# Performance work log

Hardware: AMD Instinct MI355X
Metric: run time of the kernel (lower is better)

The kernel has to match this reference:

```python
import jax, jax.numpy as jnp
import numpy as np

B, S, D, H, DFF = 4, 2048, 1024, 8, 4096
DH = D // H  # 128
EPS = 1e-5


def layernorm(x, gamma, beta):
    mu = jnp.mean(x, axis=-1, keepdims=True)
    var = jnp.mean(jnp.square(x - mu), axis=-1, keepdims=True)
    return (x - mu) * jax.lax.rsqrt(var + EPS) * gamma + beta


def setup_inputs() -> dict:
    key = jax.random.key(0)
    ks = jax.random.split(key, 6)
    s = 0.02
    return {
        "src": jax.random.normal(ks[0], (B, S, D), jnp.float32),
        "w_qkv": jax.random.normal(ks[1], (D, 3 * D), jnp.float32) * s,
        "w_out": jax.random.normal(ks[2], (D, D), jnp.float32) * s,
        "w1": jax.random.normal(ks[3], (D, DFF), jnp.float32) * s,
        "b1": jnp.zeros((DFF,), jnp.float32),
        "w2": jax.random.normal(ks[4], (DFF, D), jnp.float32) * s,
        "b2": jnp.zeros((D,), jnp.float32),
        "g1": jnp.ones((D,), jnp.float32),
        "beta1": jnp.zeros((D,), jnp.float32),
        "g2": jnp.ones((D,), jnp.float32),
        "beta2": jnp.zeros((D,), jnp.float32),
    }


def reference(src, w_qkv, w_out, w1, b1, w2, b2, g1, beta1, g2, beta2):
    b, s, d = src.shape
    # --- RingAttention == exact causal MHA on a single device ---
    qkv = src @ w_qkv  # [b, s, 3d]
    q, k, v = jnp.split(qkv, 3, axis=-1)
    to_heads = lambda x: x.reshape(b, s, H, DH).transpose(0, 2, 1, 3)  # [b,h,s,dh]
    q, k, v = to_heads(q), to_heads(k), to_heads(v)
    scale = 1.0 / jnp.sqrt(jnp.asarray(DH, src.dtype))
    scores = jnp.einsum('bhqd,bhkd->bhqk', q, k) * scale  # [b,h,s,s]
    causal = jnp.tril(jnp.ones((s, s), bool))
    neg = jnp.asarray(jnp.finfo(src.dtype).min, src.dtype)
    scores = jnp.where(causal, scores, neg)
    attn = jax.nn.softmax(scores, axis=-1)
    o = jnp.einsum('bhqk,bhkd->bhqd', attn, v)  # [b,h,s,dh]
    o = o.transpose(0, 2, 1, 3).reshape(b, s, d) @ w_out
    # dropout layers are identity at inference
    x = layernorm(src + o, g1, beta1)
    ff = jax.nn.relu(x @ w1 + b1) @ w2 + b2
    return layernorm(x + ff, g2, beta2)
```

## Files before the change

kernel.cpp:

```cpp
#include <hip/hip_runtime.h>

typedef unsigned short u16;
typedef __attribute__((ext_vector_type(8))) short short8;
typedef __attribute__((ext_vector_type(4))) float float4v;

#define MFMA_BF16(a, b, c) __builtin_amdgcn_mfma_f32_16x16x32_bf16((a), (b), (c), 0, 0, 0)

#define B_ 4
#define S_ 2048
#define D_ 1024
#define H_ 8
#define DH_ 128
#define DFF_ 4096
#define EPS_ 1e-5f
#define ROWS_ (B_ * S_)
#define CSCALE_ 0.12751672939502f

__device__ __forceinline__ u16 f2bf(float f) {
  union { float f; unsigned u; } x; x.f = f;
  unsigned r = x.u + 0x7fffu + ((x.u >> 16) & 1u);
  return (u16)(r >> 16);
}

typedef __attribute__((address_space(1))) const unsigned int guint;
typedef __attribute__((address_space(3))) unsigned int luint;
__device__ __forceinline__ void gl2lds16(const u16* g, u16* l) {
  __builtin_amdgcn_global_load_lds((guint*)g, (luint*)l, 16, 0, 0);
}

__device__ __forceinline__ size_t tiled_off(int row, int k, int Kdim) {
  return ((size_t)(row >> 7) * (Kdim >> 5) + (k >> 5)) * 4096 +
         (size_t)((row & 127) << 5) + (k & 31);
}

__global__ void cast_tiled_kernel(const float* __restrict__ in, u16* __restrict__ out) {
  int idx = blockIdx.x * 256 + threadIdx.x;
  int g = idx * 4;
  int m = g >> 10, k = g & 1023;
  float4 v = *(const float4*)(in + (size_t)g);
  ushort4 u;
  u.x = f2bf(v.x); u.y = f2bf(v.y); u.z = f2bf(v.z); u.w = f2bf(v.w);
  *(ushort4*)(out + tiled_off(m, k, D_)) = u;
}

__global__ void transpose_cast_kernel(const float* __restrict__ in, u16* __restrict__ out,
                                      int K, int N) {
  __shared__ float t[32][33];
  int k0 = blockIdx.x * 32, n0 = blockIdx.y * 32;
  int tx = threadIdx.x & 31, ty = threadIdx.x >> 5;
  #pragma unroll
  for (int i = 0; i < 4; ++i)
    t[ty + 8 * i][tx] = in[(size_t)(k0 + ty + 8 * i) * N + n0 + tx];
  __syncthreads();
  #pragma unroll
  for (int i = 0; i < 4; ++i)
    out[(size_t)(n0 + ty + 8 * i) * K + k0 + tx] = f2bf(t[tx][ty + 8 * i]);
}

__global__ void transpose_v_kernel(const u16* __restrict__ in, u16* __restrict__ out) {
  __shared__ u16 t[32][33];
  int s0 = blockIdx.x * 32, d0 = blockIdx.y * 32, bh = blockIdx.z;
  const u16* src = in + (size_t)bh * S_ * DH_;
  u16* dst = out + (size_t)bh * DH_ * S_;
  int tx = threadIdx.x & 31, ty = threadIdx.x >> 5;
  #pragma unroll
  for (int i = 0; i < 4; ++i)
    t[ty + 8 * i][tx] = src[(size_t)(s0 + ty + 8 * i) * DH_ + d0 + tx];
  __syncthreads();
  #pragma unroll
  for (int i = 0; i < 4; ++i)
    dst[(size_t)(d0 + ty + 8 * i) * S_ + s0 + tx] = t[tx][ty + 8 * i];
}

template <int MODE, int KT>
__global__ __launch_bounds__(256) void gemm_kernel(
    const u16* __restrict__ A, const u16* __restrict__ Bt,
    const int M, const int N,
    float* __restrict__ outF, u16* __restrict__ outH, const float* __restrict__ bias,
    const float* __restrict__ resid,
    u16* __restrict__ qo, u16* __restrict__ ko, u16* __restrict__ vo) {
  __shared__ u16 Bs[2][128][32];
  const int tid = threadIdx.x;
  const int lane = tid & 63, wave = tid >> 6;
  const int quad = lane >> 4, r16 = lane & 15;
  const int wm = (wave >> 1) * 64, wn = (wave & 1) * 64;
  const int m0 = blockIdx.x * 128, n0 = blockIdx.y * 128;
  constexpr int K = KT, niter = KT >> 5;

  float4v acc[4][4];
  #pragma unroll
  for (int i = 0; i < 4; ++i)
    #pragma unroll
    for (int j = 0; j < 4; ++j) acc[i][j] = (float4v)0.0f;

  const int drow = lane >> 2, dseg = lane & 3;
  const u16* Bg0 = Bt + (size_t)(n0 + wave * 32 + drow) * K + dseg * 8;
  const u16* Bg1 = Bg0 + (size_t)16 * K;
  u16* Bl0 = &Bs[0][wave * 32][0];
  u16* Bl1 = &Bs[0][wave * 32 + 16][0];
  constexpr int bufStep = 128 * 32;

  const u16* ap[4];
  #pragma unroll
  for (int t = 0; t < 4; ++t)
    ap[t] = A + (size_t)(m0 >> 7) * niter * 4096 +
            (size_t)((wm + t * 16 + r16) << 5) + quad * 8;

  gl2lds16(Bg0, Bl0);
  gl2lds16(Bg1, Bl1);
  short8 a_cur[4], a_nxt[4];
  #pragma unroll
  for (int t = 0; t < 4; ++t) a_cur[t] = *(const short8*)(ap[t]);

  #pragma unroll 2
  for (int i = 0; i < niter; ++i) {
    __syncthreads();
    if (i + 1 < niter) {
      const int k1 = (i + 1) << 5;
      const int bo = ((i + 1) & 1) ? bufStep : 0;
      gl2lds16(Bg0 + k1, Bl0 + bo);
      gl2lds16(Bg1 + k1, Bl1 + bo);
      const size_t o = (size_t)(i + 1) * 4096;
      #pragma unroll
      for (int t = 0; t < 4; ++t) a_nxt[t] = *(const short8*)(ap[t] + o);
    }
    short8 bfv[4];
    #pragma unroll
    for (int t = 0; t < 4; ++t)
      bfv[t] = *(const short8*)&Bs[i & 1][wn + t * 16 + r16][quad * 8];
    #pragma unroll
    for (int ii = 0; ii < 4; ++ii)
      #pragma unroll
      for (int j = 0; j < 4; ++j) acc[ii][j] = MFMA_BF16(a_cur[ii], bfv[j], acc[ii][j]);
    #pragma unroll
    for (int t = 0; t < 4; ++t) a_cur[t] = a_nxt[t];
  }

  #pragma unroll
  for (int i = 0; i < 4; ++i) {
    const int rowb = m0 + wm + i * 16 + quad * 4;
    #pragma unroll
    for (int j = 0; j < 4; ++j) {
      const int col = n0 + wn + j * 16 + r16;
      #pragma unroll
      for (int rg = 0; rg < 4; ++rg) {
        float val = acc[i][j][rg];
        const int r = rowb + rg;
        if (MODE == 0) {
          const int part = col >> 10, cc = col & 1023;
          const int h = cc >> 7, dh = cc & 127;
          const int b = r >> 11, s = r & 2047;
          u16* dst = (part == 0) ? qo : (part == 1) ? ko : vo;
          if (part == 0) val *= CSCALE_;
          dst[((size_t)(b * H_ + h) * S_ + s) * DH_ + dh] = f2bf(val);
        } else if (MODE == 1) {
          val += resid[(size_t)r * N + col];
          outF[(size_t)r * N + col] = val;
        } else if (MODE == 2) {
          val += bias[col];
          val = fmaxf(val, 0.0f);
          outH[tiled_off(r, col, N)] = f2bf(val);
        } else {
          val += bias[col] + resid[(size_t)r * N + col];
          outF[(size_t)r * N + col] = val;
        }
      }
    }
  }
}

__global__ __launch_bounds__(256) void attn_kernel(
    const u16* __restrict__ Q, const u16* __restrict__ Kg,
    const u16* __restrict__ Vtg, u16* __restrict__ O) {
  __shared__ u16 Ks[64][136];
  __shared__ u16 Vt[128][72];
  __shared__ u16 Pw[4][16][72];
  const int tid = threadIdx.x;
  const int lane = tid & 63, wave = tid >> 6;
  const int quad = lane >> 4, r16 = lane & 15;
  const int pairIdx = blockIdx.x;
  const int bh = blockIdx.y;
  const size_t base = (size_t)bh * S_ * DH_;
  const size_t vtb = (size_t)bh * DH_ * S_;
  const int b = bh >> 3, h = bh & 7;

  const u16* kg0 = Kg + base + (size_t)(tid >> 4) * DH_ + (tid & 15) * 8;
  u16* ksl = &Ks[tid >> 4][(tid & 15) * 8];
  const u16* vg0 = Vtg + vtb + (size_t)(tid >> 3) * S_ + (tid & 7) * 8;
  u16* vtl = &Vt[tid >> 3][(tid & 7) * 8];

  for (int half = 0; half < 2; ++half) {
    const int qb = (half == 0) ? pairIdx : 31 - pairIdx;
    const int qr = qb * 64 + wave * 16 + r16;

    short8 aq[4];
    #pragma unroll
    for (int ks = 0; ks < 4; ++ks)
      aq[ks] = *(const short8*)(Q + base + (size_t)qr * DH_ + ks * 32 + quad * 8);

    float4v acco[8];
    #pragma unroll
    for (int i = 0; i < 8; ++i) acco[i] = (float4v)0.0f;
    float m_q = -1e30f, l_q = 0.0f;

    for (int kb = 0; kb <= qb; ++kb) {
      __syncthreads();
      #pragma unroll
      for (int i = 0; i < 4; ++i)
        *(short8*)(ksl + i * 16 * 136) =
            *(const short8*)(kg0 + (size_t)(kb * 64 + i * 16) * DH_);
      #pragma unroll
      for (int i = 0; i < 4; ++i)
        *(short8*)(vtl + i * 32 * 72) =
            *(const short8*)(vg0 + (size_t)i * 32 * S_ + kb * 64);
      __syncthreads();

      float4v accs[4];
      #pragma unroll
      for (int t = 0; t < 4; ++t) accs[t] = (float4v)0.0f;
      #pragma unroll
      for (int ks = 0; ks < 4; ++ks) {
        #pragma unroll
        for (int t = 0; t < 4; ++t) {
          short8 ak = *(const short8*)&Ks[t * 16 + r16][ks * 32 + quad * 8];
          accs[t] = MFMA_BF16(ak, aq[ks], accs[t]);
        }
      }
      if (kb == qb) {
        #pragma unroll
        for (int t = 0; t < 4; ++t)
          #pragma unroll
          for (int rg = 0; rg < 4; ++rg) {
            int kc = kb * 64 + t * 16 + quad * 4 + rg;
            if (kc > qr) accs[t][rg] = -1e30f;
          }
      }
      float mv = accs[0][0];
      #pragma unroll
      for (int t = 0; t < 4; ++t)
        #pragma unroll
        for (int rg = 0; rg < 4; ++rg) mv = fmaxf(mv, accs[t][rg]);
      mv = fmaxf(mv, __shfl_xor(mv, 16));
      mv = fmaxf(mv, __shfl_xor(mv, 32));
      const float mnew = fmaxf(m_q, mv);
      const float alpha = __builtin_amdgcn_exp2f(m_q - mnew);
      float s0 = 0.0f;
      #pragma unroll
      for (int t = 0; t < 4; ++t)
        #pragma unroll
        for (int rg = 0; rg < 4; ++rg) {
          float p = __builtin_amdgcn_exp2f(accs[t][rg] - mnew);
          accs[t][rg] = p;
          s0 += p;
        }
      s0 += __shfl_xor(s0, 16);
      s0 += __shfl_xor(s0, 32);
      l_q = l_q * alpha + s0;
      m_q = mnew;

      #pragma unroll
      for (int t = 0; t < 4; ++t) {
        union { float f; unsigned u; } c0, c1, c2, c3;
        c0.f = accs[t][0]; c1.f = accs[t][1]; c2.f = accs[t][2]; c3.f = accs[t][3];
        uint2 pk;
        pk.x = ((c0.u + 0x8000u) >> 16) | ((c1.u + 0x8000u) & 0xffff0000u);
        pk.y = ((c2.u + 0x8000u) >> 16) | ((c3.u + 0x8000u) & 0xffff0000u);
        *(uint2*)&Pw[wave][r16][t * 16 + quad * 4] = pk;
      }
      float al[4];
      #pragma unroll
      for (int rg = 0; rg < 4; ++rg) al[rg] = __shfl(alpha, quad * 4 + rg);
      #pragma unroll
      for (int nt = 0; nt < 8; ++nt)
        #pragma unroll
        for (int rg = 0; rg < 4; ++rg) acco[nt][rg] *= al[rg];
      asm volatile("s_waitcnt lgkmcnt(0)" ::: "memory");
      #pragma unroll
      for (int ks2 = 0; ks2 < 2; ++ks2) {
        short8 ap = *(const short8*)&Pw[wave][r16][ks2 * 32 + quad * 8];
        #pragma unroll
        for (int nt = 0; nt < 8; ++nt) {
          short8 bv = *(const short8*)&Vt[nt * 16 + r16][ks2 * 32 + quad * 8];
          acco[nt] = MFMA_BF16(ap, bv, acco[nt]);
        }
      }
    }

    float lr[4];
    #pragma unroll
    for (int rg = 0; rg < 4; ++rg) lr[rg] = __shfl(l_q, quad * 4 + rg);
    const int sbase = qb * 64 + wave * 16 + quad * 4;
    #pragma unroll
    for (int nt = 0; nt < 8; ++nt)
      #pragma unroll
      for (int rg = 0; rg < 4; ++rg) {
        float val = acco[nt][rg] / lr[rg];
        const int row = b * S_ + sbase + rg;
        const int col = h * DH_ + nt * 16 + r16;
        O[tiled_off(row, col, D_)] = f2bf(val);
      }
  }
}

__global__ __launch_bounds__(256) void ln_kernel(
    const float* __restrict__ a,
    const float* __restrict__ g, const float* __restrict__ be,
    float* __restrict__ xf, u16* __restrict__ xb) {
  __shared__ float red[8];
  const int row = blockIdx.x, tid = threadIdx.x;
  float4 v = ((const float4*)(a + (size_t)row * D_))[tid];
  float s = v.x + v.y + v.z + v.w;
  float q = v.x * v.x + v.y * v.y + v.z * v.z + v.w * v.w;
  #pragma unroll
  for (int m = 1; m < 64; m <<= 1) {
    s += __shfl_xor(s, m);
    q += __shfl_xor(q, m);
  }
  const int wave = tid >> 6, lane = tid & 63;
  if (lane == 0) { red[wave] = s; red[4 + wave] = q; }
  __syncthreads();
  s = red[0] + red[1] + red[2] + red[3];
  q = red[4] + red[5] + red[6] + red[7];
  const float mu = s * (1.0f / D_);
  const float var = q * (1.0f / D_) - mu * mu;
  const float inv = rsqrtf(var + EPS_);
  const float4 gg = ((const float4*)g)[tid];
  const float4 bb = ((const float4*)be)[tid];
  float4 y;
  y.x = (v.x - mu) * inv * gg.x + bb.x;
  y.y = (v.y - mu) * inv * gg.y + bb.y;
  y.z = (v.z - mu) * inv * gg.z + bb.z;
  y.w = (v.w - mu) * inv * gg.w + bb.w;
  if (xf) ((float4*)(xf + (size_t)row * D_))[tid] = y;
  if (xb) {
    ushort4 u;
    u.x = f2bf(y.x); u.y = f2bf(y.y); u.z = f2bf(y.z); u.w = f2bf(y.w);
    *(ushort4*)(xb + tiled_off(row, tid * 4, D_)) = u;
  }
}

extern "C" void kernel_launch(void* const* d_in, const int* in_sizes, int n_in,
                              void* d_out, int out_size, void* d_ws, size_t ws_size,
                              hipStream_t stream) {
  const float* src   = (const float*)d_in[0];
  const float* w_qkv = (const float*)d_in[1];
  const float* w_out = (const float*)d_in[2];
  const float* w1    = (const float*)d_in[3];
  const float* b1    = (const float*)d_in[4];
  const float* w2    = (const float*)d_in[5];
  const float* b2    = (const float*)d_in[6];
  const float* g1    = (const float*)d_in[7];
  const float* be1   = (const float*)d_in[8];
  const float* g2    = (const float*)d_in[9];
  const float* be2   = (const float*)d_in[10];
  float* out = (float*)d_out;

  char* ws = (char*)d_ws;
  size_t off = 0;
  auto alloc = [&](size_t bytes) -> void* {
    void* p = ws + off;
    off += (bytes + 255) & ~(size_t)255;
    return p;
  };
  u16* src_bf = (u16*)alloc((size_t)ROWS_ * D_ * 2);
  u16* wqkvT  = (u16*)alloc((size_t)3 * D_ * D_ * 2);
  u16* woutT  = (u16*)alloc((size_t)D_ * D_ * 2);
  u16* w1T    = (u16*)alloc((size_t)DFF_ * D_ * 2);
  u16* w2T    = (u16*)alloc((size_t)D_ * DFF_ * 2);
  u16* qbuf   = (u16*)alloc((size_t)ROWS_ * D_ * 2);
  u16* kbuf   = (u16*)alloc((size_t)ROWS_ * D_ * 2);
  u16* vbuf   = (u16*)alloc((size_t)ROWS_ * D_ * 2);
  u16* obuf   = (u16*)alloc((size_t)ROWS_ * D_ * 2);
  u16* vT     = (u16*)alloc((size_t)ROWS_ * D_ * 2);
  float* proj = (float*)alloc((size_t)ROWS_ * D_ * 4);
  float* xf   = (float*)alloc((size_t)ROWS_ * D_ * 4);
  u16* xb     = (u16*)alloc((size_t)ROWS_ * D_ * 2);
  u16* h1     = qbuf;
  float* ff   = proj;

  cast_tiled_kernel<<<ROWS_ * D_ / 4 / 256, 256, 0, stream>>>(src, src_bf);
  transpose_cast_kernel<<<dim3(D_ / 32, 3 * D_ / 32), 256, 0, stream>>>(w_qkv, wqkvT, D_, 3 * D_);
  transpose_cast_kernel<<<dim3(D_ / 32, D_ / 32), 256, 0, stream>>>(w_out, woutT, D_, D_);
  transpose_cast_kernel<<<dim3(D_ / 32, DFF_ / 32), 256, 0, stream>>>(w1, w1T, D_, DFF_);
  transpose_cast_kernel<<<dim3(DFF_ / 32, D_ / 32), 256, 0, stream>>>(w2, w2T, DFF_, D_);

  gemm_kernel<0, 1024><<<dim3(ROWS_ / 128, 3 * D_ / 128), 256, 0, stream>>>(
      src_bf, wqkvT, ROWS_, 3 * D_, nullptr, nullptr, nullptr, nullptr, qbuf, kbuf, vbuf);
  transpose_v_kernel<<<dim3(S_ / 32, DH_ / 32, B_ * H_), 256, 0, stream>>>(vbuf, vT);
  attn_kernel<<<dim3(16, B_ * H_), 256, 0, stream>>>(qbuf, kbuf, vT, obuf);
  gemm_kernel<1, 1024><<<dim3(ROWS_ / 128, D_ / 128), 256, 0, stream>>>(
      obuf, woutT, ROWS_, D_, proj, nullptr, nullptr, src, nullptr, nullptr, nullptr);
  ln_kernel<<<ROWS_, 256, 0, stream>>>(proj, g1, be1, xf, xb);
  gemm_kernel<2, 1024><<<dim3(ROWS_ / 128, DFF_ / 128), 256, 0, stream>>>(
      xb, w1T, ROWS_, DFF_, nullptr, h1, b1, nullptr, nullptr, nullptr, nullptr);
  gemm_kernel<3, 4096><<<dim3(ROWS_ / 128, D_ / 128), 256, 0, stream>>>(
      h1, w2T, ROWS_, D_, ff, nullptr, b2, xf, nullptr, nullptr, nullptr);
  ln_kernel<<<ROWS_, 256, 0, stream>>>(ff, g2, be2, out, nullptr);
}
```

Before: 555.1 us.

## Deepen GEMM K-step, add XCD-aware tile mapping, fuse V transpose and weight casts

The GEMM now processes 64-wide K chunks per iteration with a doubled LDS buffer, halving barrier count per K. Blocks are remapped with a 1D grid so that each XCD handles a contiguous range of N tiles, improving L2 reuse of weight tiles. The QKV epilogue writes V directly in transposed layout with packed 4-element stores, removing the separate transpose_v kernel. The four weight transpose-cast launches are merged into one. The larger per-iteration register footprint (8 A fragments, 8 B fragments) may reduce occupancy.

```diff
diff --git a/kernel.cpp b/kernel.cpp
--- a/kernel.cpp
+++ b/kernel.cpp
@@ -43,11 +43,20 @@
   *(ushort4*)(out + tiled_off(m, k, D_)) = u;
 }
 
-__global__ void transpose_cast_kernel(const float* __restrict__ in, u16* __restrict__ out,
-                                      int K, int N) {
+__global__ void transpose_cast4_kernel(
+    const float* __restrict__ w_qkv, const float* __restrict__ w_out,
+    const float* __restrict__ w1, const float* __restrict__ w2,
+    u16* __restrict__ o_qkv, u16* __restrict__ o_out,
+    u16* __restrict__ o_w1, u16* __restrict__ o_w2) {
   __shared__ float t[32][33];
-  int k0 = blockIdx.x * 32, n0 = blockIdx.y * 32;
-  int tx = threadIdx.x & 31, ty = threadIdx.x >> 5;
+  int id = blockIdx.x;
+  const float* in; u16* out; int K, N, bx, by;
+  if (id < 3072)      { in = w_qkv; out = o_qkv; K = 1024; N = 3072; bx = id & 31;  by = id >> 5; }
+  else if (id < 4096) { id -= 3072; in = w_out; out = o_out; K = 1024; N = 1024; bx = id & 31;  by = id >> 5; }
+  else if (id < 8192) { id -= 4096; in = w1;    out = o_w1;  K = 1024; N = 4096; bx = id & 31;  by = id >> 5; }
+  else                { id -= 8192; in = w2;    out = o_w2;  K = 4096; N = 1024; bx = id & 127; by = id >> 7; }
+  const int k0 = bx * 32, n0 = by * 32;
+  const int tx = threadIdx.x & 31, ty = threadIdx.x >> 5;
   #pragma unroll
   for (int i = 0; i < 4; ++i)
     t[ty + 8 * i][tx] = in[(size_t)(k0 + ty + 8 * i) * N + n0 + tx];
@@ -57,35 +66,24 @@
     out[(size_t)(n0 + ty + 8 * i) * K + k0 + tx] = f2bf(t[tx][ty + 8 * i]);
 }
 
-__global__ void transpose_v_kernel(const u16* __restrict__ in, u16* __restrict__ out) {
-  __shared__ u16 t[32][33];
-  int s0 = blockIdx.x * 32, d0 = blockIdx.y * 32, bh = blockIdx.z;
-  const u16* src = in + (size_t)bh * S_ * DH_;
-  u16* dst = out + (size_t)bh * DH_ * S_;
-  int tx = threadIdx.x & 31, ty = threadIdx.x >> 5;
-  #pragma unroll
-  for (int i = 0; i < 4; ++i)
-    t[ty + 8 * i][tx] = src[(size_t)(s0 + ty + 8 * i) * DH_ + d0 + tx];
-  __syncthreads();
-  #pragma unroll
-  for (int i = 0; i < 4; ++i)
-    dst[(size_t)(d0 + ty + 8 * i) * S_ + s0 + tx] = t[tx][ty + 8 * i];
-}
-
 template <int MODE, int KT>
 __global__ __launch_bounds__(256) void gemm_kernel(
-    const u16* __restrict__ A, const u16* __restrict__ Bt,
-    const int M, const int N,
+    const u16* __restrict__ A, const u16* __restrict__ Bt, const int nTiles,
     float* __restrict__ outF, u16* __restrict__ outH, const float* __restrict__ bias,
     const float* __restrict__ resid,
-    u16* __restrict__ qo, u16* __restrict__ ko, u16* __restrict__ vo) {
-  __shared__ u16 Bs[2][128][32];
+    u16* __restrict__ qo, u16* __restrict__ ko, u16* __restrict__ vTo) {
+  __shared__ u16 Bs[2][2][128][32];
   const int tid = threadIdx.x;
   const int lane = tid & 63, wave = tid >> 6;
   const int quad = lane >> 4, r16 = lane & 15;
   const int wm = (wave >> 1) * 64, wn = (wave & 1) * 64;
-  const int m0 = blockIdx.x * 128, n0 = blockIdx.y * 128;
-  constexpr int K = KT, niter = KT >> 5;
+  const int bid = blockIdx.x;
+  const int xcd = bid & 7, loc = bid >> 3;
+  const int nPerX = nTiles >> 3;
+  const int m0 = (loc & 63) * 128;
+  const int n0 = (xcd * nPerX + (loc >> 6)) * 128;
+  const int N = nTiles << 7;
+  constexpr int K = KT, niter = KT >> 6;
 
   float4v acc[4][4];
   #pragma unroll
@@ -93,47 +91,66 @@
     #pragma unroll
     for (int j = 0; j < 4; ++j) acc[i][j] = (float4v)0.0f;
 
-  const int drow = lane >> 2, dseg = lane & 3;
-  const u16* Bg0 = Bt + (size_t)(n0 + wave * 32 + drow) * K + dseg * 8;
-  const u16* Bg1 = Bg0 + (size_t)16 * K;
-  u16* Bl0 = &Bs[0][wave * 32][0];
-  u16* Bl1 = &Bs[0][wave * 32 + 16][0];
-  constexpr int bufStep = 128 * 32;
+  const int srow = lane >> 2, sseg = lane & 3;
+  const u16* Bg[4];
+  u16* Bl[4];
+  #pragma unroll
+  for (int h = 0; h < 2; ++h)
+    #pragma unroll
+    for (int g2 = 0; g2 < 2; ++g2) {
+      Bg[h * 2 + g2] = Bt + (size_t)(n0 + wave * 32 + 16 * g2 + srow) * K + h * 32 + sseg * 8;
+      Bl[h * 2 + g2] = &Bs[0][h][wave * 32 + 16 * g2][0];
+    }
+  constexpr int bufStep = 2 * 128 * 32;
 
   const u16* ap[4];
   #pragma unroll
   for (int t = 0; t < 4; ++t)
-    ap[t] = A + (size_t)(m0 >> 7) * niter * 4096 +
+    ap[t] = A + (size_t)(m0 >> 7) * (K >> 5) * 4096 +
             (size_t)((wm + t * 16 + r16) << 5) + quad * 8;
 
-  gl2lds16(Bg0, Bl0);
-  gl2lds16(Bg1, Bl1);
-  short8 a_cur[4], a_nxt[4];
-  #pragma unroll
-  for (int t = 0; t < 4; ++t) a_cur[t] = *(const short8*)(ap[t]);
+  #pragma unroll
+  for (int e = 0; e < 4; ++e) gl2lds16(Bg[e], Bl[e]);
+  short8 a_cur[8], a_nxt[8];
+  #pragma unroll
+  for (int t = 0; t < 4; ++t)
+    #pragma unroll
+    for (int h2 = 0; h2 < 2; ++h2)
+      a_cur[t * 2 + h2] = *(const short8*)(ap[t] + h2 * 4096);
 
   #pragma unroll 2
   for (int i = 0; i < niter; ++i) {
     __syncthreads();
     if (i + 1 < niter) {
-      const int k1 = (i + 1) << 5;
+      const size_t kb = (size_t)(i + 1) * 64;
       const int bo = ((i + 1) & 1) ? bufStep : 0;
-      gl2lds16(Bg0 + k1, Bl0 + bo);
-      gl2lds16(Bg1 + k1, Bl1 + bo);
-      const size_t o = (size_t)(i + 1) * 4096;
-      #pragma unroll
-      for (int t = 0; t < 4; ++t) a_nxt[t] = *(const short8*)(ap[t] + o);
+      #pragma unroll
+      for (int e = 0; e < 4; ++e) gl2lds16(Bg[e] + kb, Bl[e] + bo);
+      const size_t to = (size_t)(i + 1) * 2 * 4096;
+      #pragma unroll
+      for (int t = 0; t < 4; ++t)
+        #pragma unroll
+        for (int h2 = 0; h2 < 2; ++h2)
+          a_nxt[t * 2 + h2] = *(const short8*)(ap[t] + to + h2 * 4096);
     }
-    short8 bfv[4];
+    const u16* bb = &Bs[i & 1][0][0][0];
+    short8 bf0[4], bf1[4];
     #pragma unroll
     for (int t = 0; t < 4; ++t)
-      bfv[t] = *(const short8*)&Bs[i & 1][wn + t * 16 + r16][quad * 8];
+      bf0[t] = *(const short8*)(bb + ((wn + t * 16 + r16) << 5) + quad * 8);
+    #pragma unroll
+    for (int t = 0; t < 4; ++t)
+      bf1[t] = *(const short8*)(bb + 128 * 32 + ((wn + t * 16 + r16) << 5) + quad * 8);
     #pragma unroll
     for (int ii = 0; ii < 4; ++ii)
       #pragma unroll
-      for (int j = 0; j < 4; ++j) acc[ii][j] = MFMA_BF16(a_cur[ii], bfv[j], acc[ii][j]);
-    #pragma unroll
-    for (int t = 0; t < 4; ++t) a_cur[t] = a_nxt[t];
+      for (int j = 0; j < 4; ++j) acc[ii][j] = MFMA_BF16(a_cur[ii * 2], bf0[j], acc[ii][j]);
+    #pragma unroll
+    for (int ii = 0; ii < 4; ++ii)
+      #pragma unroll
+      for (int j = 0; j < 4; ++j) acc[ii][j] = MFMA_BF16(a_cur[ii * 2 + 1], bf1[j], acc[ii][j]);
+    #pragma unroll
+    for (int e = 0; e < 8; ++e) a_cur[e] = a_nxt[e];
   }
 
   #pragma unroll
@@ -142,27 +159,40 @@
     #pragma unroll
     for (int j = 0; j < 4; ++j) {
       const int col = n0 + wn + j * 16 + r16;
-      #pragma unroll
-      for (int rg = 0; rg < 4; ++rg) {
-        float val = acc[i][j][rg];
-        const int r = rowb + rg;
-        if (MODE == 0) {
-          const int part = col >> 10, cc = col & 1023;
-          const int h = cc >> 7, dh = cc & 127;
-          const int b = r >> 11, s = r & 2047;
-          u16* dst = (part == 0) ? qo : (part == 1) ? ko : vo;
-          if (part == 0) val *= CSCALE_;
-          dst[((size_t)(b * H_ + h) * S_ + s) * DH_ + dh] = f2bf(val);
-        } else if (MODE == 1) {
-          val += resid[(size_t)r * N + col];
-          outF[(size_t)r * N + col] = val;
-        } else if (MODE == 2) {
-          val += bias[col];
-          val = fmaxf(val, 0.0f);
-          outH[tiled_off(r, col, N)] = f2bf(val);
+      if (MODE == 0) {
+        const int part = col >> 10, cc = col & 1023;
+        const int h = cc >> 7, dh = cc & 127;
+        const int b = rowb >> 11, s = rowb & 2047;
+        if (part == 2) {
+          ushort4 pk;
+          pk.x = f2bf(acc[i][j][0]); pk.y = f2bf(acc[i][j][1]);
+          pk.z = f2bf(acc[i][j][2]); pk.w = f2bf(acc[i][j][3]);
+          *(ushort4*)&vTo[((size_t)(b * H_ + h) * DH_ + dh) * S_ + s] = pk;
         } else {
-          val += bias[col] + resid[(size_t)r * N + col];
-          outF[(size_t)r * N + col] = val;
+          u16* dst = (part == 0) ? qo : ko;
+          #pragma unroll
+          for (int rg = 0; rg < 4; ++rg) {
+            float val = acc[i][j][rg];
+            if (part == 0) val *= CSCALE_;
+            dst[((size_t)(b * H_ + h) * S_ + s + rg) * DH_ + dh] = f2bf(val);
+          }
+        }
+      } else {
+        #pragma unroll
+        for (int rg = 0; rg < 4; ++rg) {
+          float val = acc[i][j][rg];
+          const int r = rowb + rg;
+          if (MODE == 1) {
+            val += resid[(size_t)r * N + col];
+            outF[(size_t)r * N + col] = val;
+          } else if (MODE == 2) {
+            val += bias[col];
+            val = fmaxf(val, 0.0f);
+            outH[tiled_off(r, col, N)] = f2bf(val);
+          } else {
+            val += bias[col] + resid[(size_t)r * N + col];
+            outF[(size_t)r * N + col] = val;
+          }
         }
       }
     }
@@ -369,9 +399,8 @@
   u16* w2T    = (u16*)alloc((size_t)D_ * DFF_ * 2);
   u16* qbuf   = (u16*)alloc((size_t)ROWS_ * D_ * 2);
   u16* kbuf   = (u16*)alloc((size_t)ROWS_ * D_ * 2);
-  u16* vbuf   = (u16*)alloc((size_t)ROWS_ * D_ * 2);
+  u16* vT     = (u16*)alloc((size_t)ROWS_ * D_ * 2);
   u16* obuf   = (u16*)alloc((size_t)ROWS_ * D_ * 2);
-  u16* vT     = (u16*)alloc((size_t)ROWS_ * D_ * 2);
   float* proj = (float*)alloc((size_t)ROWS_ * D_ * 4);
   float* xf   = (float*)alloc((size_t)ROWS_ * D_ * 4);
   u16* xb     = (u16*)alloc((size_t)ROWS_ * D_ * 2);
@@ -379,21 +408,18 @@
   float* ff   = proj;
 
   cast_tiled_kernel<<<ROWS_ * D_ / 4 / 256, 256, 0, stream>>>(src, src_bf);
-  transpose_cast_kernel<<<dim3(D_ / 32, 3 * D_ / 32), 256, 0, stream>>>(w_qkv, wqkvT, D_, 3 * D_);
-  transpose_cast_kernel<<<dim3(D_ / 32, D_ / 32), 256, 0, stream>>>(w_out, woutT, D_, D_);
-  transpose_cast_kernel<<<dim3(D_ / 32, DFF_ / 32), 256, 0, stream>>>(w1, w1T, D_, DFF_);
-  transpose_cast_kernel<<<dim3(DFF_ / 32, D_ / 32), 256, 0, stream>>>(w2, w2T, DFF_, D_);
-
-  gemm_kernel<0, 1024><<<dim3(ROWS_ / 128, 3 * D_ / 128), 256, 0, stream>>>(
-      src_bf, wqkvT, ROWS_, 3 * D_, nullptr, nullptr, nullptr, nullptr, qbuf, kbuf, vbuf);
-  transpose_v_kernel<<<dim3(S_ / 32, DH_ / 32, B_ * H_), 256, 0, stream>>>(vbuf, vT);
+  transpose_cast4_kernel<<<12288, 256, 0, stream>>>(w_qkv, w_out, w1, w2,
+                                                    wqkvT, woutT, w1T, w2T);
+
+  gemm_kernel<0, 1024><<<1536, 256, 0, stream>>>(
+      src_bf, wqkvT, 24, nullptr, nullptr, nullptr, nullptr, qbuf, kbuf, vT);
   attn_kernel<<<dim3(16, B_ * H_), 256, 0, stream>>>(qbuf, kbuf, vT, obuf);
-  gemm_kernel<1, 1024><<<dim3(ROWS_ / 128, D_ / 128), 256, 0, stream>>>(
-      obuf, woutT, ROWS_, D_, proj, nullptr, nullptr, src, nullptr, nullptr, nullptr);
+  gemm_kernel<1, 1024><<<512, 256, 0, stream>>>(
+      obuf, woutT, 8, proj, nullptr, nullptr, src, nullptr, nullptr, nullptr);
   ln_kernel<<<ROWS_, 256, 0, stream>>>(proj, g1, be1, xf, xb);
-  gemm_kernel<2, 1024><<<dim3(ROWS_ / 128, DFF_ / 128), 256, 0, stream>>>(
-      xb, w1T, ROWS_, DFF_, nullptr, h1, b1, nullptr, nullptr, nullptr, nullptr);
-  gemm_kernel<3, 4096><<<dim3(ROWS_ / 128, D_ / 128), 256, 0, stream>>>(
-      h1, w2T, ROWS_, D_, ff, nullptr, b2, xf, nullptr, nullptr, nullptr);
+  gemm_kernel<2, 1024><<<2048, 256, 0, stream>>>(
+      xb, w1T, 32, nullptr, h1, b1, nullptr, nullptr, nullptr, nullptr);
+  gemm_kernel<3, 4096><<<512, 256, 0, stream>>>(
+      h1, w2T, 8, ff, nullptr, b2, xf, nullptr, nullptr, nullptr);
   ln_kernel<<<ROWS_, 256, 0, stream>>>(ff, g2, be2, out, nullptr);
 }
```

Result: slower. 593.8 us (+7.0%).
